# Kernel tuning notes

Hardware: AMD Instinct MI355X
Metric: run time of the kernel (lower is better)

Reference implementation:

```python
import jax, jax.numpy as jnp
import numpy as np

B, D, H, G, WR = 8192, 1024, 1024, 2, 64
URANKS = [64, 64]


def setup_inputs() -> dict:
    key = jax.random.key(0)
    ks = jax.random.split(key, 12)
    s = 0.1
    return {
        "x": jax.random.normal(ks[0], (B, D), jnp.float32),
        "h": jax.random.normal(ks[1], (B, H), jnp.float32),
        "c": jax.random.normal(ks[2], (B, H), jnp.float32),
        "dia_x": s * jax.random.normal(ks[3], (1, D), jnp.float32),
        "dia_h": s * jax.random.normal(ks[4], (1, H), jnp.float32),
        "Ux": s * jax.random.normal(ks[5], (D, WR), jnp.float32),
        "Vx": s * jax.random.normal(ks[6], (4 * H, WR), jnp.float32),
        "Uh_0": s * jax.random.normal(ks[7], (G, H // G, URANKS[0]), jnp.float32),
        "Vh_0": s * jax.random.normal(ks[8], (G, URANKS[0], 4 * (H // G)), jnp.float32),
        "Uh_1": s * jax.random.normal(ks[9], (G, H // G, URANKS[1]), jnp.float32),
        "Vh_1": s * jax.random.normal(ks[10], (G, URANKS[1], 4 * (H // G)), jnp.float32),
        "bias_x": jnp.ones((1, 4 * H), jnp.float32),
        "bias_h": jnp.ones((1, 4 * H), jnp.float32),
    }


def reference(x, h, c, dia_x, dia_h, Ux, Vx, Uh_0, Vh_0, Uh_1, Vh_1, bias_x, bias_h):
    Bn, Dn = x.shape
    Hn = h.shape[1]
    g = Uh_0.shape[0]
    Hg = Hn // g
    r0 = Uh_0.shape[2]

    # diagonal (vector-multiplication) paths, x-part zero-padded to hidden width
    vm_x = jnp.pad(dia_x * x, ((0, 0), (0, Hn - Dn)))          # [B, H]
    vm_h = dia_h * h                                           # [B, H]

    # low-rank input projection
    lowered_x = (x @ Ux) @ Vx.T                                # [B, 4H]

    # refined diagonal corrections subtracted from the low-rank outputs
    Vx4 = Vx.reshape(4, Hn, -1)[:, :Dn, :]                     # [4, D, wR]
    coef_x = jnp.sum(Ux[None, :, :] * Vx4, axis=-1)            # [4, D]
    vm_refined_x = jnp.pad(x[:, None, :] * coef_x[None], ((0, 0), (0, 0), (0, Hn - Dn))).reshape(Bn, 4 * Hn)

    Uh0f = Uh_0.reshape(Hn, r0)                                # [H, r0]
    Vh0f = jnp.transpose(Vh_0, (0, 2, 1)).reshape(4 * Hn, r0).reshape(4, Hn, r0)
    coef_h = jnp.sum(Uh0f[None, :, :] * Vh0f, axis=-1)         # [4, H]
    vm_refined_h = (h[:, None, :] * coef_h[None]).reshape(Bn, 4 * Hn)

    gx = lowered_x - vm_refined_x + bias_x
    xi, xf, xo, xn = jnp.split(gx, 4, axis=1)

    # grouped low-rank recurrent projection with cyclic group permutation
    hv = h.reshape(Bn, g, Hg)
    Uhs = [Uh_0, Uh_1]
    Vhs = [Vh_0, Vh_1]
    g_h = jnp.zeros((Bn, 4 * Hn), x.dtype)
    for i in range(g):
        idx = np.roll(np.arange(g), -i)                        # static permutation
        hp = hv[:, idx, :]                                     # [B, g, H/g]
        t = jnp.einsum('bgn,gnr->bgr', hp, Uhs[i])             # [B, g, r_i]
        t = jnp.einsum('bgr,grm->bgm', t, Vhs[i])              # [B, g, 4H/g]
        g_h = g_h + t.reshape(Bn, 4 * Hn)

    gh = g_h - vm_refined_h + bias_h
    hf, hi, hn, ho = jnp.split(gh, 4, axis=1)                  # note gate order differs from x

    base = vm_x + vm_h
    inputgate = jax.nn.sigmoid(xi + hi + base)
    forgetgate = jax.nn.sigmoid(xf + hf + base)
    outputgate = jax.nn.sigmoid(xo + ho + base)
    newgate = jnp.tanh(xn + hn + base)

    c_next = forgetgate * c + inputgate * newgate
    h_next = outputgate * jnp.tanh(c_next)
    return (h_next, c_next)
```

## Files before the change

kernel.cpp:

```cpp
#include <hip/hip_runtime.h>


typedef _Float16 half8 __attribute__((ext_vector_type(8)));
typedef _Float16 half4v __attribute__((ext_vector_type(4)));
typedef float f32x4 __attribute__((ext_vector_type(4)));

#define WS_TA    0
#define WS_TB    3145728
#define WS_U1F   6291456
#define WS_UH1F  6422528
#define WS_W2    6684672
#define WS_CX    8257536
#define WS_CH    8273920
#define WS_BB    8290304

__global__ __launch_bounds__(256) void prep_kernel(
    const float* __restrict__ Ux, const float* __restrict__ Vx,
    const float* __restrict__ Uh0, const float* __restrict__ Vh0,
    const float* __restrict__ Uh1, const float* __restrict__ Vh1,
    const float* __restrict__ dia_x, const float* __restrict__ dia_h,
    const float* __restrict__ bias_x, const float* __restrict__ bias_h,
    _Float16* __restrict__ U1f, _Float16* __restrict__ Uh1f,
    _Float16* __restrict__ W2f, float* __restrict__ cx,
    float* __restrict__ ch, float* __restrict__ bb)
{
    int e = blockIdx.x * 256 + threadIdx.x;
    if (e < 8192) {
        int lane = e & 63, ks = (e >> 6) & 31, ct = e >> 11;
        int l15 = lane & 15, quad = lane >> 4;
        half8 v8;
        #pragma unroll
        for (int jj = 0; jj < 8; ++jj) {
            int k = ks * 32 + quad * 8 + jj;
            v8[jj] = (_Float16)Ux[k * 64 + ct * 16 + l15];
        }
        *(half8*)&U1f[(size_t)e * 8] = v8;
    } else if (e < 24576) {
        int t = e - 8192;
        int lane = t & 63, ks = (t >> 6) & 15, ct = (t >> 10) & 3, j = t >> 12;
        int l15 = lane & 15, quad = lane >> 4;
        const float* src = (j & 1) ? Uh1 : Uh0;
        int g = j >> 1;
        half8 v8;
        #pragma unroll
        for (int jj = 0; jj < 8; ++jj) {
            int k = ks * 32 + quad * 8 + jj;
            v8[jj] = (_Float16)src[(g * 512 + k) * 64 + ct * 16 + l15];
        }
        *(half8*)&Uh1f[(size_t)t * 8] = v8;
    } else if (e < 122880) {
        int t = e - 24576;
        int lane = t & 63;
        int ksq  = (t >> 6) % 6;
        int ct   = (t / 384) & 63;
        int g01  = (t / 24576) & 1;
        int s    = t / 49152;
        int l15 = lane & 15, quad = lane >> 4;
        int k = ct * 16 + l15;
        int jx = s * 2 + g01;
        int m = (g01 == 0) ? (1024 + k) : k;
        half8 v8;
        #pragma unroll
        for (int jj = 0; jj < 8; ++jj) {
            int kk = ksq * 32 + quad * 8 + jj;
            int r = kk & 63, sect = kk >> 6;
            float val;
            if (sect == 0)      val = Vx[(jx * 1024 + k) * 64 + r];
            else if (sect == 1) val = Vh0[(s * 64 + r) * 2048 + m];
            else                val = Vh1[(s * 64 + r) * 2048 + m];
            v8[jj] = (_Float16)val;
        }
        *(half8*)&W2f[(size_t)t * 8] = v8;
    } else if (e < 126976) {
        int t = e - 122880; int q = t >> 10; int k = t & 1023;
        int jh = q ^ 1;
        int fh = jh * 1024 + k; int g = fh >> 11; int m = fh & 2047;
        float sx = 0.f, sh = 0.f;
        for (int r = 0; r < 64; ++r) {
            sx += Ux[k * 64 + r] * Vx[(q * 1024 + k) * 64 + r];
            sh += Uh0[k * 64 + r] * Vh0[(g * 64 + r) * 2048 + m];
        }
        cx[t] = dia_x[k] - sx;
        ch[t] = dia_h[k] - sh;
        bb[t] = bias_x[q * 1024 + k] + bias_h[jh * 1024 + k];
    }
}

__global__ __launch_bounds__(256) void s1_kernel(
    const float* __restrict__ x, const float* __restrict__ h,
    const _Float16* __restrict__ U1f, const _Float16* __restrict__ Uh1f,
    _Float16* __restrict__ Ta, _Float16* __restrict__ Tb)
{
    __shared__ __align__(16) _Float16 Ash[16][520];

    const int job = blockIdx.y;
    const int b0 = blockIdx.x * 16;
    const int tid = threadIdx.x;
    const int w = tid >> 6, l = tid & 63, l15 = l & 15, quad = l >> 4;

    f32x4 acc0 = {}, acc1 = {};
    const int nkc = (job == 0) ? 2 : 1;
    const float* src = (job == 0) ? x : h;

    for (int kc = 0; kc < nkc; ++kc) {
        const int koff = (job == 2) ? 512 : kc * 512;
        #pragma unroll
        for (int ii = 0; ii < 8; ++ii) {
            int idx = tid + ii * 256;
            int row = idx >> 7, c4 = idx & 127;
            float4 f = *(const float4*)&src[(size_t)(b0 + row) * 1024 + koff + c4 * 4];
            half4v p;
            p[0] = (_Float16)f.x; p[1] = (_Float16)f.y;
            p[2] = (_Float16)f.z; p[3] = (_Float16)f.w;
            *(half4v*)&Ash[row][c4 * 4] = p;
        }
        __syncthreads();
        if (job == 0) {
            const _Float16* bp = U1f + ((size_t)(w * 32 + kc * 16) * 64 + l) * 8;
            #pragma unroll
            for (int ks = 0; ks < 16; ++ks) {
                half8 a = *(const half8*)&Ash[l15][ks * 32 + quad * 8];
                half8 b = *(const half8*)(bp + (size_t)ks * 512);
                acc0 = __builtin_amdgcn_mfma_f32_16x16x32_f16(a, b, acc0, 0, 0, 0);
            }
        } else {
            const int j0 = (job == 1) ? 0 : 1;
            const int j1 = (job == 1) ? 3 : 2;
            const _Float16* bp0 = Uh1f + ((size_t)((j0 * 4 + w) * 16) * 64 + l) * 8;
            const _Float16* bp1 = Uh1f + ((size_t)((j1 * 4 + w) * 16) * 64 + l) * 8;
            #pragma unroll
            for (int ks = 0; ks < 16; ++ks) {
                half8 a = *(const half8*)&Ash[l15][ks * 32 + quad * 8];
                half8 b0 = *(const half8*)(bp0 + (size_t)ks * 512);
                acc0 = __builtin_amdgcn_mfma_f32_16x16x32_f16(a, b0, acc0, 0, 0, 0);
                half8 b1 = *(const half8*)(bp1 + (size_t)ks * 512);
                acc1 = __builtin_amdgcn_mfma_f32_16x16x32_f16(a, b1, acc1, 0, 0, 0);
            }
        }
        __syncthreads();
    }
    if (job == 0) {
        int col = w * 16 + l15;
        #pragma unroll
        for (int r = 0; r < 4; ++r) {
            int row = b0 + quad * 4 + r;
            _Float16 v = (_Float16)acc0[r];
            Ta[(size_t)row * 192 + col] = v;
            Tb[(size_t)row * 192 + col] = v;
        }
    } else {
        int colA = ((job == 1) ? 64 : 128) + w * 16 + l15;
        int colB = ((job == 1) ? 128 : 64) + w * 16 + l15;
        #pragma unroll
        for (int r = 0; r < 4; ++r) {
            int row = b0 + quad * 4 + r;
            Ta[(size_t)row * 192 + colA] = (_Float16)acc0[r];
            Tb[(size_t)row * 192 + colB] = (_Float16)acc1[r];
        }
    }
}

__global__ __launch_bounds__(256, 2) void s2_kernel(
    const _Float16* __restrict__ Ta, const _Float16* __restrict__ Tb,
    const _Float16* __restrict__ W2f,
    const float* __restrict__ cx, const float* __restrict__ ch,
    const float* __restrict__ bb,
    const float* __restrict__ x, const float* __restrict__ h,
    const float* __restrict__ c, float* __restrict__ out)
{
    __shared__ __align__(16) _Float16 TaSh[16][200];
    __shared__ __align__(16) _Float16 TbSh[16][200];

    const int b0 = blockIdx.x * 16;
    const int kr0 = blockIdx.y * 4;
    const int tid = threadIdx.x;
    const int w = tid >> 6, l = tid & 63, l15 = l & 15, quad = l >> 4;

    #pragma unroll
    for (int ii = 0; ii < 3; ++ii) {
        int idx = tid + ii * 256;
        int arr = idx >= 384;
        int i2 = idx - (arr ? 384 : 0);
        int row = i2 / 24, c8 = i2 % 24;
        const _Float16* src = arr ? Tb : Ta;
        _Float16* dst = arr ? &TbSh[row][c8 * 8] : &TaSh[row][c8 * 8];
        *(half8*)dst = *(const half8*)&src[(size_t)(b0 + row) * 192 + c8 * 8];
    }
    __syncthreads();

    half8 aA[6], aB[6];
    #pragma unroll
    for (int ks = 0; ks < 6; ++ks) {
        aA[ks] = *(const half8*)&TaSh[l15][ks * 32 + quad * 8];
        aB[ks] = *(const half8*)&TbSh[l15][ks * 32 + quad * 8];
    }

    const size_t laneoff = (size_t)l * 8;

    #pragma unroll 1
    for (int kr = kr0; kr < kr0 + 4; ++kr) {
        const int ctg = kr * 4 + w;
        const int k = ctg * 16 + l15;
        f32x4 acc[4] = {};
        #pragma unroll
        for (int sg = 0; sg < 4; ++sg) {
            const _Float16* bp = W2f + (size_t)((sg * 64 + ctg) * 6) * 512 + laneoff;
            #pragma unroll
            for (int ks = 0; ks < 6; ++ks) {
                half8 b = *(const half8*)(bp + (size_t)ks * 512);
                acc[sg] = __builtin_amdgcn_mfma_f32_16x16x32_f16(
                    (sg < 2) ? aA[ks] : aB[ks], b, acc[sg], 0, 0, 0);
            }
        }
        float cxi = cx[k], cxf = cx[1024 + k], cxo = cx[2048 + k], cxn = cx[3072 + k];
        float chi = ch[k], chf = ch[1024 + k], cho = ch[2048 + k], chn = ch[3072 + k];
        float bbi = bb[k], bbf = bb[1024 + k], bbo = bb[2048 + k], bbn = bb[3072 + k];
        #pragma unroll
        for (int r = 0; r < 4; ++r) {
            int row = b0 + quad * 4 + r;
            size_t off = (size_t)row * 1024 + k;
            float xv = x[off], hv = h[off], cv = c[off];
            float pi = acc[0][r] + xv * cxi + hv * chi + bbi;
            float pf = acc[1][r] + xv * cxf + hv * chf + bbf;
            float po = acc[2][r] + xv * cxo + hv * cho + bbo;
            float pn = acc[3][r] + xv * cxn + hv * chn + bbn;
            float ig = 1.f / (1.f + __expf(-pi));
            float fg = 1.f / (1.f + __expf(-pf));
            float og = 1.f / (1.f + __expf(-po));
            float e2n = __expf(2.f * pn);
            float ng = 1.f - 2.f / (e2n + 1.f);
            float cn = fg * cv + ig * ng;
            float e2c = __expf(2.f * cn);
            float tc = 1.f - 2.f / (e2c + 1.f);
            out[off] = og * tc;
            out[(size_t)8388608 + off] = cn;
        }
    }
}

extern "C" void kernel_launch(void* const* d_in, const int* in_sizes, int n_in,
                              void* d_out, int out_size, void* d_ws, size_t ws_size,
                              hipStream_t stream)
{
    const float* x      = (const float*)d_in[0];
    const float* h      = (const float*)d_in[1];
    const float* c      = (const float*)d_in[2];
    const float* dia_x  = (const float*)d_in[3];
    const float* dia_h  = (const float*)d_in[4];
    const float* Ux     = (const float*)d_in[5];
    const float* Vx     = (const float*)d_in[6];
    const float* Uh0    = (const float*)d_in[7];
    const float* Vh0    = (const float*)d_in[8];
    const float* Uh1    = (const float*)d_in[9];
    const float* Vh1    = (const float*)d_in[10];
    const float* bias_x = (const float*)d_in[11];
    const float* bias_h = (const float*)d_in[12];
    float* out = (float*)d_out;

    char* ws = (char*)d_ws;
    _Float16* TaW  = (_Float16*)(ws + WS_TA);
    _Float16* TbW  = (_Float16*)(ws + WS_TB);
    _Float16* U1f  = (_Float16*)(ws + WS_U1F);
    _Float16* Uh1f = (_Float16*)(ws + WS_UH1F);
    _Float16* W2f  = (_Float16*)(ws + WS_W2);
    float* cx = (float*)(ws + WS_CX);
    float* ch = (float*)(ws + WS_CH);
    float* bb = (float*)(ws + WS_BB);

    prep_kernel<<<496, 256, 0, stream>>>(Ux, Vx, Uh0, Vh0, Uh1, Vh1,
                                         dia_x, dia_h, bias_x, bias_h,
                                         U1f, Uh1f, W2f, cx, ch, bb);
    s1_kernel<<<dim3(512, 3), 256, 0, stream>>>(x, h, U1f, Uh1f, TaW, TbW);
    s2_kernel<<<dim3(512, 4), 256, 0, stream>>>(TaW, TbW, W2f, cx, ch, bb,
                                                x, h, c, out);
}
```

Measured before the change: 251.0 us.

## Retile s2 kernel to 32-row blocks reusing W2 loads across two row tiles

```diff
diff --git a/kernel.cpp b/kernel.cpp
--- a/kernel.cpp
+++ b/kernel.cpp
@@ -160,7 +160,7 @@
     }
 }
 
-__global__ __launch_bounds__(256, 2) void s2_kernel(
+__global__ __launch_bounds__(256, 4) void s2_kernel(
     const _Float16* __restrict__ Ta, const _Float16* __restrict__ Tb,
     const _Float16* __restrict__ W2f,
     const float* __restrict__ cx, const float* __restrict__ ch,
@@ -168,19 +168,19 @@
     const float* __restrict__ x, const float* __restrict__ h,
     const float* __restrict__ c, float* __restrict__ out)
 {
-    __shared__ __align__(16) _Float16 TaSh[16][200];
-    __shared__ __align__(16) _Float16 TbSh[16][200];
-
-    const int b0 = blockIdx.x * 16;
-    const int kr0 = blockIdx.y * 4;
+    __shared__ __align__(16) _Float16 TaSh[32][200];
+    __shared__ __align__(16) _Float16 TbSh[32][200];
+
+    const int b0 = blockIdx.x * 32;
+    const int by = blockIdx.y;
     const int tid = threadIdx.x;
     const int w = tid >> 6, l = tid & 63, l15 = l & 15, quad = l >> 4;
 
     #pragma unroll
-    for (int ii = 0; ii < 3; ++ii) {
+    for (int ii = 0; ii < 6; ++ii) {
         int idx = tid + ii * 256;
-        int arr = idx >= 384;
-        int i2 = idx - (arr ? 384 : 0);
+        int arr = idx >= 768;
+        int i2 = idx - (arr ? 768 : 0);
         int row = i2 / 24, c8 = i2 % 24;
         const _Float16* src = arr ? Tb : Ta;
         _Float16* dst = arr ? &TbSh[row][c8 * 8] : &TaSh[row][c8 * 8];
@@ -188,52 +188,56 @@
     }
     __syncthreads();
 
-    half8 aA[6], aB[6];
+    const size_t laneoff = (size_t)l * 8;
+
     #pragma unroll
-    for (int ks = 0; ks < 6; ++ks) {
-        aA[ks] = *(const half8*)&TaSh[l15][ks * 32 + quad * 8];
-        aB[ks] = *(const half8*)&TbSh[l15][ks * 32 + quad * 8];
-    }
-
-    const size_t laneoff = (size_t)l * 8;
-
-    #pragma unroll 1
-    for (int kr = kr0; kr < kr0 + 4; ++kr) {
-        const int ctg = kr * 4 + w;
+    for (int kr = 0; kr < 2; ++kr) {
+        const int ctg = by * 8 + kr * 4 + w;
         const int k = ctg * 16 + l15;
-        f32x4 acc[4] = {};
-        #pragma unroll
-        for (int sg = 0; sg < 4; ++sg) {
-            const _Float16* bp = W2f + (size_t)((sg * 64 + ctg) * 6) * 512 + laneoff;
-            #pragma unroll
-            for (int ks = 0; ks < 6; ++ks) {
-                half8 b = *(const half8*)(bp + (size_t)ks * 512);
-                acc[sg] = __builtin_amdgcn_mfma_f32_16x16x32_f16(
-                    (sg < 2) ? aA[ks] : aB[ks], b, acc[sg], 0, 0, 0);
+        f32x4 acc[4][2] = {};
+        const _Float16* bpi = W2f + (size_t)((0 * 64 + ctg) * 6) * 512 + laneoff;
+        const _Float16* bpf = W2f + (size_t)((1 * 64 + ctg) * 6) * 512 + laneoff;
+        const _Float16* bpo = W2f + (size_t)((2 * 64 + ctg) * 6) * 512 + laneoff;
+        const _Float16* bpn = W2f + (size_t)((3 * 64 + ctg) * 6) * 512 + laneoff;
+        #pragma unroll
+        for (int ks = 0; ks < 6; ++ks) {
+            half8 bi = *(const half8*)(bpi + (size_t)ks * 512);
+            half8 bf = *(const half8*)(bpf + (size_t)ks * 512);
+            half8 bo = *(const half8*)(bpo + (size_t)ks * 512);
+            half8 bn = *(const half8*)(bpn + (size_t)ks * 512);
+            #pragma unroll
+            for (int rt = 0; rt < 2; ++rt) {
+                half8 aA = *(const half8*)&TaSh[rt * 16 + l15][ks * 32 + quad * 8];
+                half8 aB = *(const half8*)&TbSh[rt * 16 + l15][ks * 32 + quad * 8];
+                acc[0][rt] = __builtin_amdgcn_mfma_f32_16x16x32_f16(aA, bi, acc[0][rt], 0, 0, 0);
+                acc[1][rt] = __builtin_amdgcn_mfma_f32_16x16x32_f16(aA, bf, acc[1][rt], 0, 0, 0);
+                acc[2][rt] = __builtin_amdgcn_mfma_f32_16x16x32_f16(aB, bo, acc[2][rt], 0, 0, 0);
+                acc[3][rt] = __builtin_amdgcn_mfma_f32_16x16x32_f16(aB, bn, acc[3][rt], 0, 0, 0);
             }
         }
         float cxi = cx[k], cxf = cx[1024 + k], cxo = cx[2048 + k], cxn = cx[3072 + k];
         float chi = ch[k], chf = ch[1024 + k], cho = ch[2048 + k], chn = ch[3072 + k];
         float bbi = bb[k], bbf = bb[1024 + k], bbo = bb[2048 + k], bbn = bb[3072 + k];
         #pragma unroll
-        for (int r = 0; r < 4; ++r) {
-            int row = b0 + quad * 4 + r;
-            size_t off = (size_t)row * 1024 + k;
-            float xv = x[off], hv = h[off], cv = c[off];
-            float pi = acc[0][r] + xv * cxi + hv * chi + bbi;
-            float pf = acc[1][r] + xv * cxf + hv * chf + bbf;
-            float po = acc[2][r] + xv * cxo + hv * cho + bbo;
-            float pn = acc[3][r] + xv * cxn + hv * chn + bbn;
-            float ig = 1.f / (1.f + __expf(-pi));
-            float fg = 1.f / (1.f + __expf(-pf));
-            float og = 1.f / (1.f + __expf(-po));
-            float e2n = __expf(2.f * pn);
-            float ng = 1.f - 2.f / (e2n + 1.f);
-            float cn = fg * cv + ig * ng;
-            float e2c = __expf(2.f * cn);
-            float tc = 1.f - 2.f / (e2c + 1.f);
-            out[off] = og * tc;
-            out[(size_t)8388608 + off] = cn;
+        for (int rt = 0; rt < 2; ++rt) {
+            #pragma unroll
+            for (int r = 0; r < 4; ++r) {
+                int row = b0 + rt * 16 + quad * 4 + r;
+                size_t off = (size_t)row * 1024 + k;
+                float xv = x[off], hv = h[off], cv = c[off];
+                float pi = acc[0][rt][r] + xv * cxi + hv * chi + bbi;
+                float pf = acc[1][rt][r] + xv * cxf + hv * chf + bbf;
+                float po = acc[2][rt][r] + xv * cxo + hv * cho + bbo;
+                float pn = acc[3][rt][r] + xv * cxn + hv * chn + bbn;
+                float ig = __builtin_amdgcn_rcpf(1.f + __expf(-pi));
+                float fg = __builtin_amdgcn_rcpf(1.f + __expf(-pf));
+                float og = __builtin_amdgcn_rcpf(1.f + __expf(-po));
+                float ng = 1.f - 2.f * __builtin_amdgcn_rcpf(__expf(2.f * pn) + 1.f);
+                float cn = fg * cv + ig * ng;
+                float tc = 1.f - 2.f * __builtin_amdgcn_rcpf(__expf(2.f * cn) + 1.f);
+                out[off] = og * tc;
+                out[(size_t)8388608 + off] = cn;
+            }
         }
     }
 }
@@ -271,6 +275,6 @@
                                          dia_x, dia_h, bias_x, bias_h,
                                          U1f, Uh1f, W2f, cx, ch, bb);
     s1_kernel<<<dim3(512, 3), 256, 0, stream>>>(x, h, U1f, Uh1f, TaW, TbW);
-    s2_kernel<<<dim3(512, 4), 256, 0, stream>>>(TaW, TbW, W2f, cx, ch, bb,
+    s2_kernel<<<dim3(256, 8), 256, 0, stream>>>(TaW, TbW, W2f, cx, ch, bb,
                                                 x, h, c, out);
 }
```

Result: faster. 244.6 us (-2.6%).
